# Kernel tuning notes

Measured on AMD Instinct MI355X. Metric: run time of the kernel, lower is better.

Reference implementation:

```python
import jax, jax.numpy as jnp
import numpy as np

N, M, H, C = 20000, 20000, 32, 128
KP_EXTENT = 0.6
EPS = 1e-5


def _kpconv(q_pts, s_pts, neighb_inds, x, kernel_points, weights):
    """Rigid KPConv, linear influence, 'sum' aggregation, Predator-style density norm."""
    # shadow point / shadow feature padding (index M is the shadow slot)
    s_pad = jnp.concatenate([s_pts, jnp.full((1, 3), 1e6, s_pts.dtype)], axis=0)
    x_pad = jnp.concatenate([x, jnp.zeros((1, x.shape[1]), x.dtype)], axis=0)
    neighbors = s_pad[neighb_inds] - q_pts[:, None, :]              # [N,H,3]
    diff = neighbors[:, :, None, :] - kernel_points[None, None]      # [N,H,K,3]
    sq = jnp.sum(diff * diff, axis=-1)                               # [N,H,K]
    dist = jnp.sqrt(jnp.maximum(sq, 1e-12))
    all_weights = jnp.clip(1.0 - dist / KP_EXTENT, 0.0, None)        # linear KP influence
    neighb_x = x_pad[neighb_inds]                                    # [N,H,C]
    weighted = jnp.einsum('nhk,nhc->nkc', all_weights, neighb_x)     # [N,K,C]
    out = jnp.einsum('nkc,kcd->nd', weighted, weights)               # [N,D]
    # density normalization by number of valid neighbors
    feat_sum = jnp.sum(neighb_x, axis=-1)                            # [N,H]
    n_num = jnp.maximum(jnp.sum(feat_sum > 0.0, axis=-1), 1)         # [N]
    return out / n_num[:, None].astype(out.dtype)


def _segment_norm(x, len0):
    """Per-cloud (instance) normalization over stacked points, 2 clouds, no affine."""
    n = x.shape[0]
    seg = (jnp.arange(n) >= len0).astype(jnp.int32)                  # [N] in {0,1}
    onehot = jax.nn.one_hot(seg, 2, dtype=x.dtype)                   # [N,2]
    cnt = jnp.maximum(onehot.sum(axis=0), 1.0)                       # [2]
    mean = (onehot.T @ x) / cnt[:, None]                             # [2,C]
    var = (onehot.T @ (x * x)) / cnt[:, None] - mean * mean          # [2,C]
    return (x - mean[seg]) * jax.lax.rsqrt(var[seg] + EPS)


def _batchnorm1d(x, gamma, beta):
    mean = jnp.mean(x, axis=0)
    var = jnp.mean(x * x, axis=0) - mean * mean                      # biased, as torch BN
    return (x - mean) * jax.lax.rsqrt(var + EPS) * gamma + beta


def _rand_kernel_points(key, k, radius):
    pts = jax.random.normal(key, (k, 3), dtype=jnp.float32)
    pts = pts / jnp.linalg.norm(pts, axis=1, keepdims=True)
    r = jax.random.uniform(jax.random.fold_in(key, 1), (k, 1)) ** (1.0 / 3.0)
    return pts * r * radius


def setup_inputs() -> dict:
    key = jax.random.key(0)
    ks = jax.random.split(key, 10)
    D = C // 2  # 64, per-branch out channels
    q_pts = jax.random.uniform(ks[0], (N, 3), dtype=jnp.float32)
    s_pts = jax.random.uniform(ks[1], (M, 3), dtype=jnp.float32)
    neighb_inds = jax.random.randint(ks[2], (N, H), 0, M)
    x = jax.random.normal(ks[3], (M, C), dtype=jnp.float32)
    stack_lengths_post = jnp.array([N // 2, N - N // 2], dtype=jnp.int32)
    kp_mini = _rand_kernel_points(ks[4], 7, 1.0 * 1.5)               # radius * 1.5
    w_mini = jax.random.normal(ks[5], (7, C, D), dtype=jnp.float32) * (1.0 / np.sqrt(C))
    kp_mid = _rand_kernel_points(ks[6], 13, 1.0)                      # radius
    w_mid = jax.random.normal(ks[7], (13, C, D), dtype=jnp.float32) * (1.0 / np.sqrt(C))
    w_midmini = jax.random.normal(ks[8], (D, D), dtype=jnp.float32) * (1.0 / np.sqrt(D))
    w_final = jax.random.normal(ks[9], (C, C), dtype=jnp.float32) * (1.0 / np.sqrt(C))
    gamma_final = jnp.ones((C,), jnp.float32)
    beta_final = jnp.zeros((C,), jnp.float32)
    return dict(q_pts=q_pts, s_pts=s_pts, neighb_inds=neighb_inds, x=x,
                stack_lengths_post=stack_lengths_post,
                kp_mini=kp_mini, w_mini=w_mini, kp_mid=kp_mid, w_mid=w_mid,
                w_midmini=w_midmini, w_final=w_final,
                gamma_final=gamma_final, beta_final=beta_final)


def reference(q_pts, s_pts, neighb_inds, x, stack_lengths_post,
              kp_mini, w_mini, kp_mid, w_mid, w_midmini, w_final,
              gamma_final, beta_final):
    len0 = stack_lengths_post[0]
    x1 = _kpconv(q_pts, s_pts, neighb_inds, x, kp_mini, w_mini)      # [N, C//2]
    x1 = _segment_norm(x1, len0)
    x2 = _kpconv(q_pts, s_pts, neighb_inds, x, kp_mid, w_mid)        # [N, C//2]
    x2 = _segment_norm(x2, len0)
    x2 = (x1 + x2) @ w_midmini.T                                     # nn.Linear(bias=False)
    xc = jnp.concatenate([x1, x2], axis=1)                           # [N, C]
    out = xc @ w_final.T
    out = _batchnorm1d(out, gamma_final, beta_final)
    return jax.nn.relu(out)
```

## Files before the change

kernel.cpp:

```cpp
#include <hip/hip_runtime.h>
#include <math.h>

#define NQ 20000
#define MS 20000
#define HN 32
#define CH 128
#define DH 64
#define KTOT 20
#define KMINI 7
#define EPSN 1e-5f
#define KDIM 2560
#define NKT 80
#define NMT 1250
#define KT_Y1 28

#define OFF_ROWSUM 0
#define OFF_Y1     20480
#define OFF_Y2     (OFF_Y1 + NQ*DH)
#define OFF_SEGSUM (OFF_Y2 + NQ*DH)
#define OFF_BNSUM  (OFF_SEGSUM + 512)
#define OFF_BNSQ   (OFF_BNSUM + 128)
#define OFF_OUTPRE (OFF_BNSQ + 128)
#define OFF_WSWZ   (OFF_OUTPRE + NQ*CH)
#define OFF_CFRAG  (OFF_WSWZ + 163840)
#define OFF_P      (OFF_CFRAG + 8192)
#define TOT_FLOATS (OFF_P + NQ*KDIM/2)

typedef __attribute__((ext_vector_type(8))) short bf16x8;
typedef __attribute__((ext_vector_type(4))) float f32x4;
typedef __attribute__((ext_vector_type(4))) unsigned short us4;

static __device__ inline unsigned short f2bf(float f) {
    unsigned int u = __float_as_uint(f);
    unsigned int r = (u + 0x7fffu + ((u >> 16) & 1u)) >> 16;
    return (unsigned short)r;
}

__global__ __launch_bounds__(256) void k_prep(
    const float* __restrict__ x, float* __restrict__ rowsum,
    const float* __restrict__ w_mini, const float* __restrict__ w_mid,
    const float* __restrict__ w_midmini, const float* __restrict__ w_final,
    unsigned short* __restrict__ wswz, unsigned short* __restrict__ cfrag)
{
    if (blockIdx.x < 5000) {
        int row = blockIdx.x * 4 + (threadIdx.x >> 6);
        int lane = threadIdx.x & 63;
        if (row >= MS) return;
        double s = (double)x[row * CH + lane] + (double)x[row * CH + 64 + lane];
        #pragma unroll
        for (int off = 32; off > 0; off >>= 1) s += __shfl_down(s, off, 64);
        if (lane == 0) rowsum[row] = (float)s;
    } else if (blockIdx.x < 6280) {
        int gid = (blockIdx.x - 5000) * 256 + threadIdx.x;
        if (gid >= NKT * 8 * 512) return;
        int j = gid & 7;
        int l = (gid >> 3) & 63;
        int ntkt = gid >> 9;
        int nt = ntkt & 7;
        int kt = ntkt >> 3;
        int kg = kt * 32 + ((l >> 4) << 3) + j;
        int d  = nt * 16 + (l & 15);
        int k = kg >> 7, c = kg & 127;
        float v = 0.0f;
        if (k < KMINI && d < DH)        v = w_mini[((size_t)k * CH + c) * DH + d];
        else if (k >= KMINI && d >= DH) v = w_mid[((size_t)(k - KMINI) * CH + c) * DH + (d - DH)];
        wswz[gid] = f2bf(v);
    } else {
        int b2 = blockIdx.x - 6280;
        int kt = b2 >> 3, nt = b2 & 7;
        for (int e = threadIdx.x; e < 512; e += 256) {
            int l = e >> 3, j = e & 7;
            int i = kt * 32 + ((l >> 4) << 3) + j;
            int jcol = nt * 16 + (l & 15);
            const float* wfr = &w_final[(size_t)jcol * 128 + 64];
            int ec = i & 63;
            float dsum = 0.f;
            #pragma unroll 8
            for (int dd = 0; dd < 64; ++dd)
                dsum += w_midmini[dd * 64 + ec] * wfr[dd];
            float cv = dsum + ((i < 64) ? w_final[(size_t)jcol * 128 + i] : 0.f);
            cfrag[(size_t)(kt * 8 + nt) * 512 + e] = f2bf(cv);
        }
    }
}

__global__ __launch_bounds__(256) void k_gather(
    const float* __restrict__ q_pts, const float* __restrict__ s_pts,
    const int* __restrict__ inds, const float* __restrict__ x,
    const float* __restrict__ kp_mini, const float* __restrict__ kp_mid,
    const float* __restrict__ rowsum,
    unsigned short* __restrict__ P)
{
    __shared__ __align__(16) float kpts[KTOT][3];
    __shared__ __align__(16) float nb[256][3];
    __shared__ int   nidx[256];
    __shared__ int   vcnt[8];
    __shared__ float winv[8];
    __shared__ __align__(16) float wts[8][HN][KTOT];

    const int t = threadIdx.x;
    const int n0 = blockIdx.x * 8;

    if (t < KTOT * 3) {
        int k = t / 3, j = t % 3;
        kpts[k][j] = (k < KMINI) ? kp_mini[k * 3 + j] : kp_mid[(k - KMINI) * 3 + j];
    }
    if (t < 8) vcnt[t] = 0;
    __syncthreads();

    {
        int r = t >> 5, h = t & 31;
        int n = n0 + r;
        int idx = inds[n * HN + h];
        nidx[t] = idx;
        float qx = q_pts[n * 3 + 0], qy = q_pts[n * 3 + 1], qz = q_pts[n * 3 + 2];
        nb[t][0] = s_pts[idx * 3 + 0] - qx;
        nb[t][1] = s_pts[idx * 3 + 1] - qy;
        nb[t][2] = s_pts[idx * 3 + 2] - qz;
        if (rowsum[idx] > 0.0f) atomicAdd(&vcnt[r], 1);
    }
    __syncthreads();
    if (t < 8) winv[t] = 1.0f / (float)max(vcnt[t], 1);
    __syncthreads();

    for (int tt = t; tt < 8 * HN * KTOT; tt += 256) {
        int r = tt / (HN * KTOT);
        int rem = tt % (HN * KTOT);
        int h = rem / KTOT, k = rem % KTOT;
        float dx = nb[r * HN + h][0] - kpts[k][0];
        float dy = nb[r * HN + h][1] - kpts[k][1];
        float dz = nb[r * HN + h][2] - kpts[k][2];
        float sq = dx * dx + dy * dy + dz * dz;
        float dist = sqrtf(fmaxf(sq, 1e-12f));
        float w = fmaxf(1.0f - dist * (1.0f / 0.6f), 0.0f);
        wts[r][h][k] = w * winv[r];
    }
    __syncthreads();

    const int r = t >> 5;
    const int c4 = t & 31;
    float acc[KTOT][4];
    #pragma unroll
    for (int k = 0; k < KTOT; ++k) {
        acc[k][0] = 0.f; acc[k][1] = 0.f; acc[k][2] = 0.f; acc[k][3] = 0.f;
    }
    const float* wbase = &wts[r][0][0];
    const int* nid = &nidx[r * HN];
    #pragma unroll 2
    for (int h = 0; h < HN; ++h) {
        int idx = nid[h];
        float4 xv = *(const float4*)&x[(size_t)idx * CH + c4 * 4];
        const float4* wp = (const float4*)(wbase + h * KTOT);
        float warr[20];
        *(float4*)&warr[0]  = wp[0];
        *(float4*)&warr[4]  = wp[1];
        *(float4*)&warr[8]  = wp[2];
        *(float4*)&warr[12] = wp[3];
        *(float4*)&warr[16] = wp[4];
        #pragma unroll
        for (int k = 0; k < KTOT; ++k) {
            float wv = warr[k];
            acc[k][0] += wv * xv.x; acc[k][1] += wv * xv.y;
            acc[k][2] += wv * xv.z; acc[k][3] += wv * xv.w;
        }
    }
    const int n = n0 + r;
    const int mt = n >> 4, m15 = n & 15;
    const int lq = (c4 & 7) >> 1;
    const int l = lq * 16 + m15;
    const int j = (c4 & 1) * 4;
    #pragma unroll
    for (int k = 0; k < KTOT; ++k) {
        int kt = k * 4 + (c4 >> 3);
        us4 v;
        v[0] = f2bf(acc[k][0]); v[1] = f2bf(acc[k][1]);
        v[2] = f2bf(acc[k][2]); v[3] = f2bf(acc[k][3]);
        *(us4*)(P + ((size_t)mt * NKT + kt) * 512 + l * 8 + j) = v;
    }
}

__global__ __launch_bounds__(256) void k_mfma(
    const unsigned short* __restrict__ P, const unsigned short* __restrict__ wswz,
    const int* __restrict__ stacklen,
    float* __restrict__ y1, float* __restrict__ y2, float* __restrict__ segsum)
{
    const int t = threadIdx.x;
    const int l = t & 63;
    const int w = t >> 6;
    const int chunk = blockIdx.y;
    const int mt = blockIdx.x * 4 + w;
    if (mt >= NMT) return;
    const int kb = chunk ? KT_Y1 : 0;
    const int ke = chunk ? NKT : KT_Y1;
    const int ntb = chunk ? 4 : 0;

    f32x4 acc[4];
    #pragma unroll
    for (int q = 0; q < 4; ++q) acc[q] = (f32x4){0.f, 0.f, 0.f, 0.f};

    const unsigned short* ap = P + (size_t)mt * NKT * 512 + l * 8;
    const unsigned short* bp = wswz + l * 8;

    #pragma unroll 2
    for (int kt = kb; kt < ke; ++kt) {
        bf16x8 a = *(const bf16x8*)(ap + (size_t)kt * 512);
        #pragma unroll
        for (int q = 0; q < 4; ++q) {
            bf16x8 b = *(const bf16x8*)(bp + (size_t)((kt * 8) + ntb + q) * 512);
            acc[q] = __builtin_amdgcn_mfma_f32_16x16x32_bf16(a, b, acc[q], 0, 0, 0);
        }
    }

    const int len0 = stacklen[0];
    float* yb = chunk ? y2 : y1;
    const int quad = l >> 4, c16 = l & 15;
    const int base_sum = (chunk * 2) * 2 * 64;

    bool all0 = (mt * 16 + 15 < len0);
    bool all1 = (mt * 16 >= len0);
    #pragma unroll
    for (int q = 0; q < 4; ++q) {
        float s0 = 0.f, q0 = 0.f, s1 = 0.f, q1 = 0.f;
        #pragma unroll
        for (int reg = 0; reg < 4; ++reg) {
            int row = mt * 16 + quad * 4 + reg;
            float v = acc[q][reg];
            yb[(size_t)row * DH + q * 16 + c16] = v;
            if (row < len0) { s0 += v; q0 += v * v; }
            else            { s1 += v; q1 += v * v; }
        }
        s0 += __shfl_xor(s0, 16); s0 += __shfl_xor(s0, 32);
        q0 += __shfl_xor(q0, 16); q0 += __shfl_xor(q0, 32);
        s1 += __shfl_xor(s1, 16); s1 += __shfl_xor(s1, 32);
        q1 += __shfl_xor(q1, 16); q1 += __shfl_xor(q1, 32);
        if (quad == 0) {
            int ch = q * 16 + c16;
            if (!all1) {
                atomicAdd(&segsum[base_sum + 0 * 64 + ch], s0);
                atomicAdd(&segsum[base_sum + 1 * 64 + ch], q0);
            }
            if (!all0) {
                atomicAdd(&segsum[base_sum + 2 * 64 + ch], s1);
                atomicAdd(&segsum[base_sum + 3 * 64 + ch], q1);
            }
        }
    }
}

__global__ __launch_bounds__(128) void k_tailmm(
    const float* __restrict__ y1, const float* __restrict__ y2,
    const float* __restrict__ segsum, const int* __restrict__ stacklen,
    const unsigned short* __restrict__ cfrag,
    float* __restrict__ outpre, float* __restrict__ bnsum, float* __restrict__ bnsq)
{
    __shared__ __align__(16) unsigned short alds[32 * 136];
    __shared__ float sstat[4][2][64];
    const int t = threadIdx.x;
    const int mb = blockIdx.x * 32;
    const int len0 = stacklen[0];

    for (int tt = t; tt < 256; tt += 128) {
        int combo = tt >> 6, ch = tt & 63;
        float cnt = (float)max((combo & 1) ? (NQ - len0) : len0, 1);
        float S = segsum[(combo * 2 + 0) * 64 + ch];
        float Q = segsum[(combo * 2 + 1) * 64 + ch];
        float mean = S / cnt;
        float var = Q / cnt - mean * mean;
        sstat[combo][0][ch] = mean;
        sstat[combo][1][ch] = rsqrtf(fmaxf(var, 0.f) + EPSN);
    }
    __syncthreads();

    for (int tt = t; tt < 32 * 32; tt += 128) {
        int r = tt >> 5, c4 = tt & 31;
        int n = mb + r;
        us4 v4 = (us4){0, 0, 0, 0};
        if (n < NQ) {
            int s = (n >= len0) ? 1 : 0;
            int c = c4 * 4;
            if (c < 64) {
                float4 yv = *(const float4*)&y1[(size_t)n * DH + c];
                v4[0] = f2bf((yv.x - sstat[s][0][c + 0]) * sstat[s][1][c + 0]);
                v4[1] = f2bf((yv.y - sstat[s][0][c + 1]) * sstat[s][1][c + 1]);
                v4[2] = f2bf((yv.z - sstat[s][0][c + 2]) * sstat[s][1][c + 2]);
                v4[3] = f2bf((yv.w - sstat[s][0][c + 3]) * sstat[s][1][c + 3]);
            } else {
                int c2 = c - 64;
                float4 yv = *(const float4*)&y2[(size_t)n * DH + c2];
                v4[0] = f2bf((yv.x - sstat[2 + s][0][c2 + 0]) * sstat[2 + s][1][c2 + 0]);
                v4[1] = f2bf((yv.y - sstat[2 + s][0][c2 + 1]) * sstat[2 + s][1][c2 + 1]);
                v4[2] = f2bf((yv.z - sstat[2 + s][0][c2 + 2]) * sstat[2 + s][1][c2 + 2]);
                v4[3] = f2bf((yv.w - sstat[2 + s][0][c2 + 3]) * sstat[2 + s][1][c2 + 3]);
            }
        }
        *(us4*)(alds + r * 136 + c4 * 4) = v4;
    }
    __syncthreads();

    const int l = t & 63, w = t >> 6;
    f32x4 acc[8];
    #pragma unroll
    for (int q = 0; q < 8; ++q) acc[q] = (f32x4){0.f, 0.f, 0.f, 0.f};

    const unsigned short* ap = alds + (w * 16 + (l & 15)) * 136 + ((l >> 4) << 3);
    const unsigned short* bp = cfrag + l * 8;
    #pragma unroll
    for (int kt = 0; kt < 4; ++kt) {
        bf16x8 a = *(const bf16x8*)(ap + kt * 32);
        #pragma unroll
        for (int nt = 0; nt < 8; ++nt) {
            bf16x8 b = *(const bf16x8*)(bp + (size_t)((kt * 8 + nt) << 9));
            acc[nt] = __builtin_amdgcn_mfma_f32_16x16x32_bf16(a, b, acc[nt], 0, 0, 0);
        }
    }

    const int quad = l >> 4, c16 = l & 15;
    #pragma unroll
    for (int nt = 0; nt < 8; ++nt) {
        float s = 0.f, q = 0.f;
        #pragma unroll
        for (int reg = 0; reg < 4; ++reg) {
            int row = mb + w * 16 + quad * 4 + reg;
            float v = acc[nt][reg];
            if (row < NQ) outpre[(size_t)row * CH + nt * 16 + c16] = v;
            else v = 0.f;
            s += v; q += v * v;
        }
        s += __shfl_xor(s, 16); s += __shfl_xor(s, 32);
        q += __shfl_xor(q, 16); q += __shfl_xor(q, 32);
        if (quad == 0) {
            atomicAdd(&bnsum[nt * 16 + c16], s);
            atomicAdd(&bnsq[nt * 16 + c16], q);
        }
    }
}

__global__ __launch_bounds__(256) void k_kpconv(
    const float* __restrict__ q_pts, const float* __restrict__ s_pts,
    const int* __restrict__ inds, const float* __restrict__ x,
    const float* __restrict__ kp_mini, const float* __restrict__ kp_mid,
    const float* __restrict__ w_mini, const float* __restrict__ w_mid,
    const float* __restrict__ rowsum,
    float* __restrict__ y1, float* __restrict__ y2)
{
    __shared__ __align__(16) float kpts[KTOT][3];
    __shared__ __align__(16) float nb[128][3];
    __shared__ int   nidx[128];
    __shared__ int   vcnt[4];
    __shared__ float winv[4];
    __shared__ __align__(16) float wts[4][HN][KTOT];
    __shared__ __align__(16) float wt[KTOT][CH][4];
    __shared__ __align__(16) float part[128][4];

    const int t = threadIdx.x;
    const int n0 = blockIdx.x * 4;

    if (t < KTOT * 3) {
        int k = t / 3, j = t % 3;
        kpts[k][j] = (k < KMINI) ? kp_mini[k * 3 + j] : kp_mid[(k - KMINI) * 3 + j];
    }
    if (t < 4) vcnt[t] = 0;
    __syncthreads();

    if (t < 128) {
        int r = t >> 5, h = t & 31;
        int n = n0 + r;
        int idx = inds[n * HN + h];
        nidx[t] = idx;
        float qx = q_pts[n * 3 + 0], qy = q_pts[n * 3 + 1], qz = q_pts[n * 3 + 2];
        nb[t][0] = s_pts[idx * 3 + 0] - qx;
        nb[t][1] = s_pts[idx * 3 + 1] - qy;
        nb[t][2] = s_pts[idx * 3 + 2] - qz;
        if (rowsum[idx] > 0.0f) atomicAdd(&vcnt[r], 1);
    }
    __syncthreads();
    if (t < 4) winv[t] = 1.0f / (float)max(vcnt[t], 1);
    __syncthreads();

    for (int tt = t; tt < 4 * HN * KTOT; tt += 256) {
        int r = tt / (HN * KTOT);
        int rem = tt % (HN * KTOT);
        int h = rem / KTOT, k = rem % KTOT;
        float dx = nb[r * HN + h][0] - kpts[k][0];
        float dy = nb[r * HN + h][1] - kpts[k][1];
        float dz = nb[r * HN + h][2] - kpts[k][2];
        float sq = dx * dx + dy * dy + dz * dz;
        float dist = sqrtf(fmaxf(sq, 1e-12f));
        float w = fmaxf(1.0f - dist * (1.0f / 0.6f), 0.0f);
        wts[r][h][k] = w * winv[r];
    }
    __syncthreads();

    {
        const int g = t >> 7;
        const int c = t & 127;
        for (int rr = 0; rr < 2; ++rr) {
            const int r = g + rr * 2;
            float acc[KTOT];
            #pragma unroll
            for (int k = 0; k < KTOT; ++k) acc[k] = 0.0f;
            for (int h = 0; h < HN; ++h) {
                int idx = nidx[r * HN + h];
                float xv = x[(size_t)idx * CH + c];
                const float4* wp = (const float4*)&wts[r][h][0];
                float4 wa = wp[0], wb = wp[1], wc = wp[2], wd = wp[3], we = wp[4];
                acc[0]  += wa.x * xv; acc[1]  += wa.y * xv; acc[2]  += wa.z * xv; acc[3]  += wa.w * xv;
                acc[4]  += wb.x * xv; acc[5]  += wb.y * xv; acc[6]  += wb.z * xv; acc[7]  += wb.w * xv;
                acc[8]  += wc.x * xv; acc[9]  += wc.y * xv; acc[10] += wc.z * xv; acc[11] += wc.w * xv;
                acc[12] += wd.x * xv; acc[13] += wd.y * xv; acc[14] += wd.z * xv; acc[15] += wd.w * xv;
                acc[16] += we.x * xv; acc[17] += we.y * xv; acc[18] += we.z * xv; acc[19] += we.w * xv;
            }
            #pragma unroll
            for (int k = 0; k < KTOT; ++k) wt[k][c][r] = acc[k];
        }
    }
    __syncthreads();

    {
        const int d = t & 127;
        const int half = t >> 7;
        const int c0 = half * 64;
        float o0 = 0.f, o1 = 0.f, o2 = 0.f, o3 = 0.f;
        if (d < DH) {
            for (int k = 0; k < KMINI; ++k) {
                const float* wp = &w_mini[((size_t)k * CH + c0) * DH + d];
                for (int c = c0; c < c0 + 64; ++c) {
                    float wv = *wp; wp += DH;
                    const float4 wtv = *(const float4*)&wt[k][c][0];
                    o0 += wv * wtv.x; o1 += wv * wtv.y; o2 += wv * wtv.z; o3 += wv * wtv.w;
                }
            }
        } else {
            const int dd = d - DH;
            for (int k = KMINI; k < KTOT; ++k) {
                const float* wp = &w_mid[((size_t)(k - KMINI) * CH + c0) * DH + dd];
                for (int c = c0; c < c0 + 64; ++c) {
                    float wv = *wp; wp += DH;
                    const float4 wtv = *(const float4*)&wt[k][c][0];
                    o0 += wv * wtv.x; o1 += wv * wtv.y; o2 += wv * wtv.z; o3 += wv * wtv.w;
                }
            }
        }
        if (half == 1) { part[d][0] = o0; part[d][1] = o1; part[d][2] = o2; part[d][3] = o3; }
        __syncthreads();
        if (half == 0) {
            o0 += part[d][0]; o1 += part[d][1]; o2 += part[d][2]; o3 += part[d][3];
            if (d < DH) {
                y1[(size_t)(n0 + 0) * DH + d] = o0;
                y1[(size_t)(n0 + 1) * DH + d] = o1;
                y1[(size_t)(n0 + 2) * DH + d] = o2;
                y1[(size_t)(n0 + 3) * DH + d] = o3;
            } else {
                const int dd = d - DH;
                y2[(size_t)(n0 + 0) * DH + dd] = o0;
                y2[(size_t)(n0 + 1) * DH + dd] = o1;
                y2[(size_t)(n0 + 2) * DH + dd] = o2;
                y2[(size_t)(n0 + 3) * DH + dd] = o3;
            }
        }
    }
}

__global__ __launch_bounds__(256) void k_segpart(
    const float* __restrict__ y1, const float* __restrict__ y2,
    const int* __restrict__ stacklen, float* __restrict__ segsum)
{
    const int t = threadIdx.x;
    const int ch = t & 63, grp = t >> 6;
    const int len0 = stacklen[0];
    float a0 = 0.f, a1 = 0.f, a2 = 0.f, a3 = 0.f;
    float b0 = 0.f, b1 = 0.f, b2 = 0.f, b3 = 0.f;
    for (int r = blockIdx.x * 4 + grp; r < NQ; r += 256 * 4) {
        float v1 = y1[(size_t)r * DH + ch];
        float v2 = y2[(size_t)r * DH + ch];
        bool in1 = (r >= len0);
        float m0 = in1 ? 0.f : 1.f, m1 = 1.f - m0;
        a0 += m0 * v1; a1 += m0 * v1 * v1; a2 += m1 * v1; a3 += m1 * v1 * v1;
        b0 += m0 * v2; b1 += m0 * v2 * v2; b2 += m1 * v2; b3 += m1 * v2 * v2;
    }
    __shared__ float red[4][8][64];
    red[grp][0][ch] = a0; red[grp][1][ch] = a1; red[grp][2][ch] = a2; red[grp][3][ch] = a3;
    red[grp][4][ch] = b0; red[grp][5][ch] = b1; red[grp][6][ch] = b2; red[grp][7][ch] = b3;
    __syncthreads();
    for (int tt = t; tt < 512; tt += 256) {
        int j = tt >> 6, c = tt & 63;
        float s = red[0][j][c] + red[1][j][c] + red[2][j][c] + red[3][j][c];
        atomicAdd(&segsum[j * 64 + c], s);
    }
}

__global__ __launch_bounds__(256) void k_tail(
    const float* __restrict__ y1, const float* __restrict__ y2,
    const float* __restrict__ segsum, const int* __restrict__ stacklen,
    const float* __restrict__ w_midmini, const float* __restrict__ w_final,
    float* __restrict__ outpre, float* __restrict__ bnsum, float* __restrict__ bnsq)
{
    __shared__ __align__(16) float sstat[4][2][64];
    __shared__ __align__(16) float sbuf[8][64];
    __shared__ __align__(16) float xc[8][128];
    __shared__ float lsum[2][128], lsq[2][128];
    const int n0 = blockIdx.x * 8;
    const int t = threadIdx.x;
    const int len0 = stacklen[0];

    {
        int combo = t >> 6, ch = t & 63;
        float cnt = (float)max((combo & 1) ? (NQ - len0) : len0, 1);
        float S = segsum[(combo * 2 + 0) * 64 + ch];
        float Q = segsum[(combo * 2 + 1) * 64 + ch];
        float mean = S / cnt;
        float var = Q / cnt - mean * mean;
        sstat[combo][0][ch] = mean;
        sstat[combo][1][ch] = rsqrtf(fmaxf(var, 0.f) + EPSN);
    }
    __syncthreads();

    for (int tt = t; tt < 8 * 64; tt += 256) {
        int r = tt >> 6, d = tt & 63;
        int n = n0 + r;
        int s = (n >= len0) ? 1 : 0;
        float x1n = (y1[(size_t)n * DH + d] - sstat[s][0][d]) * sstat[s][1][d];
        float x2n = (y2[(size_t)n * DH + d] - sstat[2 + s][0][d]) * sstat[2 + s][1][d];
        xc[r][d] = x1n;
        sbuf[r][d] = x1n + x2n;
    }
    __syncthreads();

    for (int tt = t; tt < 8 * 64; tt += 256) {
        int r = tt >> 6, d = tt & 63;
        float a = 0.f;
        const float4* wmr = (const float4*)&w_midmini[(size_t)d * 64];
        const float4* sv = (const float4*)&sbuf[r][0];
        #pragma unroll
        for (int e4 = 0; e4 < 16; ++e4) {
            float4 w4 = wmr[e4], s4 = sv[e4];
            a += w4.x * s4.x + w4.y * s4.y + w4.z * s4.z + w4.w * s4.w;
        }
        xc[r][64 + d] = a;
    }
    __syncthreads();

    {
        const int j = t & 127;
        const int g = t >> 7;
        float o0 = 0.f, o1 = 0.f, o2 = 0.f, o3 = 0.f;
        const float4* wfr = (const float4*)&w_final[(size_t)j * 128];
        #pragma unroll 8
        for (int i4 = 0; i4 < 32; ++i4) {
            float4 wf = wfr[i4];
            float4 a0 = *(const float4*)&xc[g + 0][i4 * 4];
            float4 a1 = *(const float4*)&xc[g + 2][i4 * 4];
            float4 a2 = *(const float4*)&xc[g + 4][i4 * 4];
            float4 a3 = *(const float4*)&xc[g + 6][i4 * 4];
            o0 += wf.x * a0.x + wf.y * a0.y + wf.z * a0.z + wf.w * a0.w;
            o1 += wf.x * a1.x + wf.y * a1.y + wf.z * a1.z + wf.w * a1.w;
            o2 += wf.x * a2.x + wf.y * a2.y + wf.z * a2.z + wf.w * a2.w;
            o3 += wf.x * a3.x + wf.y * a3.y + wf.z * a3.z + wf.w * a3.w;
        }
        outpre[(size_t)(n0 + g + 0) * CH + j] = o0;
        outpre[(size_t)(n0 + g + 2) * CH + j] = o1;
        outpre[(size_t)(n0 + g + 4) * CH + j] = o2;
        outpre[(size_t)(n0 + g + 6) * CH + j] = o3;
        lsum[g][j] = o0 + o1 + o2 + o3;
        lsq[g][j]  = o0 * o0 + o1 * o1 + o2 * o2 + o3 * o3;
        __syncthreads();
        if (g == 0) {
            atomicAdd(&bnsum[j], lsum[0][j] + lsum[1][j]);
            atomicAdd(&bnsq[j],  lsq[0][j] + lsq[1][j]);
        }
    }
}

__global__ __launch_bounds__(256) void k_bnapply(const float* __restrict__ outpre,
    const float* __restrict__ bnsum, const float* __restrict__ bnsq,
    const float* __restrict__ gamma, const float* __restrict__ beta,
    float* __restrict__ out)
{
    int e4 = blockIdx.x * 256 + threadIdx.x;
    if (e4 >= NQ * CH / 4) return;
    int j0 = (e4 * 4) & 127;
    float4 v = ((const float4*)outpre)[e4];
    float vv[4] = {v.x, v.y, v.z, v.w};
    float res[4];
    #pragma unroll
    for (int i = 0; i < 4; ++i) {
        int j = j0 + i;
        float mean = bnsum[j] * (1.0f / NQ);
        float var = bnsq[j] * (1.0f / NQ) - mean * mean;
        float rstd = rsqrtf(fmaxf(var, 0.f) + EPSN);
        float r = (vv[i] - mean) * rstd * gamma[j] + beta[j];
        res[i] = fmaxf(r, 0.f);
    }
    ((float4*)out)[e4] = make_float4(res[0], res[1], res[2], res[3]);
}

extern "C" void kernel_launch(void* const* d_in, const int* in_sizes, int n_in,
                              void* d_out, int out_size, void* d_ws, size_t ws_size,
                              hipStream_t stream) {
    const float* q_pts     = (const float*)d_in[0];
    const float* s_pts     = (const float*)d_in[1];
    const int*   inds      = (const int*)d_in[2];
    const float* x         = (const float*)d_in[3];
    const int*   stacklen  = (const int*)d_in[4];
    const float* kp_mini   = (const float*)d_in[5];
    const float* w_mini    = (const float*)d_in[6];
    const float* kp_mid    = (const float*)d_in[7];
    const float* w_mid     = (const float*)d_in[8];
    const float* w_midmini = (const float*)d_in[9];
    const float* w_final   = (const float*)d_in[10];
    const float* gamma     = (const float*)d_in[11];
    const float* beta      = (const float*)d_in[12];

    float* ws      = (float*)d_ws;
    float* rowsum  = ws + OFF_ROWSUM;
    float* y1      = ws + OFF_Y1;
    float* y2      = ws + OFF_Y2;
    float* segsum  = ws + OFF_SEGSUM;
    float* bnsum   = ws + OFF_BNSUM;
    float* bnsq    = ws + OFF_BNSQ;
    float* outpre  = ws + OFF_OUTPRE;
    unsigned short* wswz  = (unsigned short*)(ws + OFF_WSWZ);
    unsigned short* cfrag = (unsigned short*)(ws + OFF_CFRAG);
    unsigned short* P     = (unsigned short*)(ws + OFF_P);

    hipMemsetAsync(segsum, 0, 768 * sizeof(float), stream);

    if (ws_size >= (size_t)TOT_FLOATS * sizeof(float)) {
        k_prep<<<5000 + 1280 + 32, 256, 0, stream>>>(x, rowsum, w_mini, w_mid,
                                                     w_midmini, w_final, wswz, cfrag);
        k_gather<<<NQ / 8, 256, 0, stream>>>(q_pts, s_pts, inds, x, kp_mini, kp_mid,
                                             rowsum, P);
        dim3 mg((NMT + 3) / 4, 2);
        k_mfma<<<mg, 256, 0, stream>>>(P, wswz, stacklen, y1, y2, segsum);
        k_tailmm<<<(NQ + 31) / 32, 128, 0, stream>>>(y1, y2, segsum, stacklen, cfrag,
                                                     outpre, bnsum, bnsq);
    } else {
        k_prep<<<5000, 256, 0, stream>>>(x, rowsum, w_mini, w_mid,
                                         w_midmini, w_final, wswz, cfrag);
        k_kpconv<<<NQ / 4, 256, 0, stream>>>(q_pts, s_pts, inds, x, kp_mini, kp_mid,
                                             w_mini, w_mid, rowsum, y1, y2);
        k_segpart<<<256, 256, 0, stream>>>(y1, y2, stacklen, segsum);
        k_tail<<<NQ / 8, 256, 0, stream>>>(y1, y2, segsum, stacklen, w_midmini, w_final,
                                           outpre, bnsum, bnsq);
    }

    k_bnapply<<<(NQ * CH / 4 + 255) / 256, 256, 0, stream>>>(outpre, bnsum, bnsq,
                                                             gamma, beta, (float*)d_out);
}
```

Before: 261.0 us.

## Fuse neighbor gather and weight GEMM into one MFMA kernel without P buffer

Merges the gather and weighted-sum kernel with the large bf16 GEMM kernel. Each block of 16 query points builds the kernel-point weights as MFMA fragments, computes the [K,C] intermediate in shared memory with MFMA instead of scalar FMAs, and immediately multiplies it by the swizzled weight matrix. This removes the ~100MB bf16 P intermediate write and reread and one launch. In exchange it adds more syncs, higher shared-memory use per block, fewer blocks, and repeated wswz loads per block from cache.

```diff
diff --git a/kernel.cpp b/kernel.cpp
--- a/kernel.cpp
+++ b/kernel.cpp
@@ -9,9 +9,7 @@
 #define KTOT 20
 #define KMINI 7
 #define EPSN 1e-5f
-#define KDIM 2560
 #define NKT 80
-#define NMT 1250
 #define KT_Y1 28
 
 #define OFF_ROWSUM 0
@@ -23,8 +21,10 @@
 #define OFF_OUTPRE (OFF_BNSQ + 128)
 #define OFF_WSWZ   (OFF_OUTPRE + NQ*CH)
 #define OFF_CFRAG  (OFF_WSWZ + 163840)
-#define OFF_P      (OFF_CFRAG + 8192)
-#define TOT_FLOATS (OFF_P + NQ*KDIM/2)
+#define TOT_FLOATS (OFF_CFRAG + 8192)
+
+#define PK 40
+#define PQ 840
 
 typedef __attribute__((ext_vector_type(8))) short bf16x8;
 typedef __attribute__((ext_vector_type(4))) float f32x4;
@@ -84,148 +84,148 @@
     }
 }
 
-__global__ __launch_bounds__(256) void k_gather(
+__global__ __launch_bounds__(256) void k_fused2(
     const float* __restrict__ q_pts, const float* __restrict__ s_pts,
     const int* __restrict__ inds, const float* __restrict__ x,
     const float* __restrict__ kp_mini, const float* __restrict__ kp_mid,
-    const float* __restrict__ rowsum,
-    unsigned short* __restrict__ P)
+    const float* __restrict__ rowsum, const unsigned short* __restrict__ wswz,
+    const int* __restrict__ stacklen,
+    float* __restrict__ y1, float* __restrict__ y2, float* __restrict__ segsum)
 {
-    __shared__ __align__(16) float kpts[KTOT][3];
-    __shared__ __align__(16) float nb[256][3];
-    __shared__ int   nidx[256];
-    __shared__ int   vcnt[8];
-    __shared__ float winv[8];
-    __shared__ __align__(16) float wts[8][HN][KTOT];
+    __shared__ __align__(16) char pool[36096];
+    unsigned short* Pt = (unsigned short*)pool;
+    unsigned short* xg = (unsigned short*)(pool + 26880);
+    float* nbv = (float*)pool;
+    __shared__ int nidx[512];
+    __shared__ float kpts[KTOT][3];
+    __shared__ int vcnt[16];
+    __shared__ float winv[16];
 
     const int t = threadIdx.x;
-    const int n0 = blockIdx.x * 8;
+    const int l = t & 63;
+    const int w = t >> 6;
+    const int c16 = l & 15;
+    const int quad = l >> 4;
+    const int n0 = blockIdx.x * 16;
 
     if (t < KTOT * 3) {
         int k = t / 3, j = t % 3;
         kpts[k][j] = (k < KMINI) ? kp_mini[k * 3 + j] : kp_mid[(k - KMINI) * 3 + j];
     }
-    if (t < 8) vcnt[t] = 0;
-    __syncthreads();
-
-    {
-        int r = t >> 5, h = t & 31;
+    if (t < 16) vcnt[t] = 0;
+    __syncthreads();
+
+    for (int tt = t; tt < 512; tt += 256) {
+        int r = tt >> 5, h = tt & 31;
         int n = n0 + r;
         int idx = inds[n * HN + h];
-        nidx[t] = idx;
+        nidx[tt] = idx;
         float qx = q_pts[n * 3 + 0], qy = q_pts[n * 3 + 1], qz = q_pts[n * 3 + 2];
-        nb[t][0] = s_pts[idx * 3 + 0] - qx;
-        nb[t][1] = s_pts[idx * 3 + 1] - qy;
-        nb[t][2] = s_pts[idx * 3 + 2] - qz;
+        nbv[tt * 3 + 0] = s_pts[idx * 3 + 0] - qx;
+        nbv[tt * 3 + 1] = s_pts[idx * 3 + 1] - qy;
+        nbv[tt * 3 + 2] = s_pts[idx * 3 + 2] - qz;
         if (rowsum[idx] > 0.0f) atomicAdd(&vcnt[r], 1);
     }
     __syncthreads();
-    if (t < 8) winv[t] = 1.0f / (float)max(vcnt[t], 1);
-    __syncthreads();
-
-    for (int tt = t; tt < 8 * HN * KTOT; tt += 256) {
-        int r = tt / (HN * KTOT);
-        int rem = tt % (HN * KTOT);
-        int h = rem / KTOT, k = rem % KTOT;
-        float dx = nb[r * HN + h][0] - kpts[k][0];
-        float dy = nb[r * HN + h][1] - kpts[k][1];
-        float dz = nb[r * HN + h][2] - kpts[k][2];
-        float sq = dx * dx + dy * dy + dz * dz;
-        float dist = sqrtf(fmaxf(sq, 1e-12f));
-        float w = fmaxf(1.0f - dist * (1.0f / 0.6f), 0.0f);
-        wts[r][h][k] = w * winv[r];
-    }
-    __syncthreads();
-
-    const int r = t >> 5;
-    const int c4 = t & 31;
-    float acc[KTOT][4];
+    if (t < 16) winv[t] = 1.0f / (float)max(vcnt[t], 1);
+    __syncthreads();
+
+    bf16x8 aw0[4], aw1[4];
+    const float k0x = kpts[c16][0], k0y = kpts[c16][1], k0z = kpts[c16][2];
+    const bool v1 = (c16 < 4);
+    const float k1x = v1 ? kpts[16 + c16][0] : 0.f;
+    const float k1y = v1 ? kpts[16 + c16][1] : 0.f;
+    const float k1z = v1 ? kpts[16 + c16][2] : 0.f;
     #pragma unroll
-    for (int k = 0; k < KTOT; ++k) {
-        acc[k][0] = 0.f; acc[k][1] = 0.f; acc[k][2] = 0.f; acc[k][3] = 0.f;
-    }
-    const float* wbase = &wts[r][0][0];
-    const int* nid = &nidx[r * HN];
-    #pragma unroll 2
-    for (int h = 0; h < HN; ++h) {
-        int idx = nid[h];
-        float4 xv = *(const float4*)&x[(size_t)idx * CH + c4 * 4];
-        const float4* wp = (const float4*)(wbase + h * KTOT);
-        float warr[20];
-        *(float4*)&warr[0]  = wp[0];
-        *(float4*)&warr[4]  = wp[1];
-        *(float4*)&warr[8]  = wp[2];
-        *(float4*)&warr[12] = wp[3];
-        *(float4*)&warr[16] = wp[4];
+    for (int s = 0; s < 4; ++s) {
+        const int qi = w * 4 + s;
+        const float wi = winv[qi];
+        const float* nvb = nbv + (qi * 32 + quad * 8) * 3;
+        #pragma unroll
+        for (int j = 0; j < 8; ++j) {
+            float bx = nvb[j * 3 + 0], by = nvb[j * 3 + 1], bz = nvb[j * 3 + 2];
+            float dx = bx - k0x, dy = by - k0y, dz = bz - k0z;
+            float d = sqrtf(fmaxf(dx * dx + dy * dy + dz * dz, 1e-12f));
+            aw0[s][j] = (short)f2bf(fmaxf(1.0f - d * (1.0f / 0.6f), 0.0f) * wi);
+            if (v1) {
+                dx = bx - k1x; dy = by - k1y; dz = bz - k1z;
+                d = sqrtf(fmaxf(dx * dx + dy * dy + dz * dz, 1e-12f));
+                aw1[s][j] = (short)f2bf(fmaxf(1.0f - d * (1.0f / 0.6f), 0.0f) * wi);
+            } else {
+                aw1[s][j] = 0;
+            }
+        }
+    }
+    __syncthreads();
+
+    f32x4 accY1 = (f32x4){0.f, 0.f, 0.f, 0.f};
+    f32x4 accY2 = (f32x4){0.f, 0.f, 0.f, 0.f};
+    unsigned short* xgw = xg + w * (32 * 36);
+    const f32x4 zero4 = (f32x4){0.f, 0.f, 0.f, 0.f};
+
+    for (int ktc = 0; ktc < 4; ++ktc) {
+        #pragma unroll
+        for (int s = 0; s < 4; ++s) {
+            const int qi = w * 4 + s;
+            #pragma unroll
+            for (int i = 0; i < 4; ++i) {
+                int gid = i * 64 + l;
+                int h = gid >> 3, c4i = gid & 7;
+                int idx = nidx[qi * 32 + h];
+                float4 xv = *(const float4*)&x[(size_t)idx * CH + ktc * 32 + c4i * 4];
+                us4 v;
+                v[0] = f2bf(xv.x); v[1] = f2bf(xv.y); v[2] = f2bf(xv.z); v[3] = f2bf(xv.w);
+                *(us4*)&xgw[h * 36 + c4i * 4] = v;
+            }
+            asm volatile("s_waitcnt lgkmcnt(0)" ::: "memory");
+            #pragma unroll
+            for (int cf = 0; cf < 2; ++cf) {
+                bf16x8 bb;
+                #pragma unroll
+                for (int j = 0; j < 8; ++j)
+                    bb[j] = (short)xgw[(quad * 8 + j) * 36 + cf * 16 + c16];
+                f32x4 d0 = __builtin_amdgcn_mfma_f32_16x16x32_bf16(aw0[s], bb, zero4, 0, 0, 0);
+                f32x4 d1 = __builtin_amdgcn_mfma_f32_16x16x32_bf16(aw1[s], bb, zero4, 0, 0, 0);
+                unsigned short* pq = Pt + qi * PQ + cf * 16 + c16;
+                #pragma unroll
+                for (int reg = 0; reg < 4; ++reg)
+                    pq[(quad * 4 + reg) * PK] = f2bf(d0[reg]);
+                if (quad == 0) {
+                    #pragma unroll
+                    for (int reg = 0; reg < 4; ++reg)
+                        pq[(16 + reg) * PK] = f2bf(d1[reg]);
+                }
+            }
+        }
+        __syncthreads();
+
         #pragma unroll
         for (int k = 0; k < KTOT; ++k) {
-            float wv = warr[k];
-            acc[k][0] += wv * xv.x; acc[k][1] += wv * xv.y;
-            acc[k][2] += wv * xv.z; acc[k][3] += wv * xv.w;
-        }
-    }
-    const int n = n0 + r;
-    const int mt = n >> 4, m15 = n & 15;
-    const int lq = (c4 & 7) >> 1;
-    const int l = lq * 16 + m15;
-    const int j = (c4 & 1) * 4;
+            int ktg = k * 4 + ktc;
+            bf16x8 a = *(const bf16x8*)&Pt[c16 * PQ + k * PK + quad * 8];
+            int nt = (k < KMINI) ? w : 4 + w;
+            bf16x8 b = *(const bf16x8*)&wswz[((size_t)(ktg * 8 + nt) << 9) + l * 8];
+            if (k < KMINI) accY1 = __builtin_amdgcn_mfma_f32_16x16x32_bf16(a, b, accY1, 0, 0, 0);
+            else           accY2 = __builtin_amdgcn_mfma_f32_16x16x32_bf16(a, b, accY2, 0, 0, 0);
+        }
+        __syncthreads();
+    }
+
+    const int len0 = stacklen[0];
+    const bool all0 = (n0 + 15 < len0);
+    const bool all1 = (n0 >= len0);
+    const int ch = w * 16 + c16;
     #pragma unroll
-    for (int k = 0; k < KTOT; ++k) {
-        int kt = k * 4 + (c4 >> 3);
-        us4 v;
-        v[0] = f2bf(acc[k][0]); v[1] = f2bf(acc[k][1]);
-        v[2] = f2bf(acc[k][2]); v[3] = f2bf(acc[k][3]);
-        *(us4*)(P + ((size_t)mt * NKT + kt) * 512 + l * 8 + j) = v;
-    }
-}
-
-__global__ __launch_bounds__(256) void k_mfma(
-    const unsigned short* __restrict__ P, const unsigned short* __restrict__ wswz,
-    const int* __restrict__ stacklen,
-    float* __restrict__ y1, float* __restrict__ y2, float* __restrict__ segsum)
-{
-    const int t = threadIdx.x;
-    const int l = t & 63;
-    const int w = t >> 6;
-    const int chunk = blockIdx.y;
-    const int mt = blockIdx.x * 4 + w;
-    if (mt >= NMT) return;
-    const int kb = chunk ? KT_Y1 : 0;
-    const int ke = chunk ? NKT : KT_Y1;
-    const int ntb = chunk ? 4 : 0;
-
-    f32x4 acc[4];
-    #pragma unroll
-    for (int q = 0; q < 4; ++q) acc[q] = (f32x4){0.f, 0.f, 0.f, 0.f};
-
-    const unsigned short* ap = P + (size_t)mt * NKT * 512 + l * 8;
-    const unsigned short* bp = wswz + l * 8;
-
-    #pragma unroll 2
-    for (int kt = kb; kt < ke; ++kt) {
-        bf16x8 a = *(const bf16x8*)(ap + (size_t)kt * 512);
-        #pragma unroll
-        for (int q = 0; q < 4; ++q) {
-            bf16x8 b = *(const bf16x8*)(bp + (size_t)((kt * 8) + ntb + q) * 512);
-            acc[q] = __builtin_amdgcn_mfma_f32_16x16x32_bf16(a, b, acc[q], 0, 0, 0);
-        }
-    }
-
-    const int len0 = stacklen[0];
-    float* yb = chunk ? y2 : y1;
-    const int quad = l >> 4, c16 = l & 15;
-    const int base_sum = (chunk * 2) * 2 * 64;
-
-    bool all0 = (mt * 16 + 15 < len0);
-    bool all1 = (mt * 16 >= len0);
-    #pragma unroll
-    for (int q = 0; q < 4; ++q) {
+    for (int half = 0; half < 2; ++half) {
+        f32x4 acc = half ? accY2 : accY1;
+        float* yb = half ? y2 : y1;
+        const int sbase = half ? 256 : 0;
         float s0 = 0.f, q0 = 0.f, s1 = 0.f, q1 = 0.f;
         #pragma unroll
         for (int reg = 0; reg < 4; ++reg) {
-            int row = mt * 16 + quad * 4 + reg;
-            float v = acc[q][reg];
-            yb[(size_t)row * DH + q * 16 + c16] = v;
+            int row = n0 + quad * 4 + reg;
+            float v = acc[reg];
+            yb[(size_t)row * DH + ch] = v;
             if (row < len0) { s0 += v; q0 += v * v; }
             else            { s1 += v; q1 += v * v; }
         }
@@ -234,14 +234,13 @@
         s1 += __shfl_xor(s1, 16); s1 += __shfl_xor(s1, 32);
         q1 += __shfl_xor(q1, 16); q1 += __shfl_xor(q1, 32);
         if (quad == 0) {
-            int ch = q * 16 + c16;
             if (!all1) {
-                atomicAdd(&segsum[base_sum + 0 * 64 + ch], s0);
-                atomicAdd(&segsum[base_sum + 1 * 64 + ch], q0);
+                atomicAdd(&segsum[sbase + 0 * 64 + ch], s0);
+                atomicAdd(&segsum[sbase + 1 * 64 + ch], q0);
             }
             if (!all0) {
-                atomicAdd(&segsum[base_sum + 2 * 64 + ch], s1);
-                atomicAdd(&segsum[base_sum + 3 * 64 + ch], q1);
+                atomicAdd(&segsum[sbase + 2 * 64 + ch], s1);
+                atomicAdd(&segsum[sbase + 3 * 64 + ch], q1);
             }
         }
     }
@@ -621,17 +620,14 @@
     float* outpre  = ws + OFF_OUTPRE;
     unsigned short* wswz  = (unsigned short*)(ws + OFF_WSWZ);
     unsigned short* cfrag = (unsigned short*)(ws + OFF_CFRAG);
-    unsigned short* P     = (unsigned short*)(ws + OFF_P);
 
     hipMemsetAsync(segsum, 0, 768 * sizeof(float), stream);
 
     if (ws_size >= (size_t)TOT_FLOATS * sizeof(float)) {
         k_prep<<<5000 + 1280 + 32, 256, 0, stream>>>(x, rowsum, w_mini, w_mid,
                                                      w_midmini, w_final, wswz, cfrag);
-        k_gather<<<NQ / 8, 256, 0, stream>>>(q_pts, s_pts, inds, x, kp_mini, kp_mid,
-                                             rowsum, P);
-        dim3 mg((NMT + 3) / 4, 2);
-        k_mfma<<<mg, 256, 0, stream>>>(P, wswz, stacklen, y1, y2, segsum);
+        k_fused2<<<NQ / 16, 256, 0, stream>>>(q_pts, s_pts, inds, x, kp_mini, kp_mid,
+                                              rowsum, wswz, stacklen, y1, y2, segsum);
         k_tailmm<<<(NQ + 31) / 32, 128, 0, stream>>>(y1, y2, segsum, stacklen, cfrag,
                                                      outpre, bnsum, bnsq);
     } else {
```

Result: faster. 232.6 us (-10.9%).
